# Performance work log

Hardware: AMD Instinct MI355X
Metric: run time of the kernel (lower is better)

## Reference

```python
import jax, jax.numpy as jnp
import numpy as np

N, E, H, NUM_RBF = 50000, 800000, 32, 32
D_IN = 2 * (NUM_RBF + H)  # 128: att_src(H) + att_dst(H) + rbf(2*NUM_RBF)
LN_EPS = 1e-5


def _decompose(t):
    # irreducible decomposition of [..., 3, 3] tensor
    eye = jnp.eye(3, dtype=t.dtype)
    I = jnp.mean(jnp.diagonal(t, axis1=-2, axis2=-1), axis=-1)[..., None, None] * eye
    A = 0.5 * (t - jnp.swapaxes(t, -1, -2))
    S = 0.5 * (t + jnp.swapaxes(t, -1, -2)) - I
    return I, A, S


def _tnorm(t):
    # squared Frobenius norm over last two dims -> [..., H]
    return (t ** 2).sum((-2, -1))


def _chan_lin(t, W):
    # nn.Linear over channel dim: t [N,H,3,3], W [H_out,H_in]
    return jnp.einsum('nhij,gh->ngij', t, W)


def setup_inputs() -> dict:
    key = jax.random.key(0)
    ks = jax.random.split(key, 12)

    def lin(k, o, i):
        return (jax.random.normal(k, (o, i), jnp.float32) / np.sqrt(i)).astype(jnp.float32)

    return {
        'X': jax.random.normal(ks[0], (N, H, 3, 3), jnp.float32),
        'rbf': jax.random.normal(ks[1], (E, 2 * NUM_RBF), jnp.float32),
        'dist': jax.random.uniform(ks[2], (E,), jnp.float32),
        'src': jax.random.randint(ks[3], (E,), 0, N),
        'dst': jax.random.randint(ks[4], (E,), 0, N),
        'Ws0': lin(ks[5], H, D_IN), 'b0': jnp.zeros((H,), jnp.float32),
        'Ws1': lin(ks[6], 2 * H, H), 'b1': jnp.zeros((2 * H,), jnp.float32),
        'Ws2': lin(ks[7], 3 * H, 2 * H), 'b2': jnp.zeros((3 * H,), jnp.float32),
        'Wt': (jax.random.normal(ks[8], (6, H, H), jnp.float32) / np.sqrt(H)).astype(jnp.float32),
        'ln_w': jnp.ones((3 * H,), jnp.float32), 'ln_b': jnp.zeros((3 * H,), jnp.float32),
        'lin_w': lin(ks[9], H, 3 * H), 'lin_b': jnp.zeros((H,), jnp.float32),
    }


def reference(X, rbf, dist, src, dst, Ws0, b0, Ws1, b1, Ws2, b2, Wt, ln_w, ln_b, lin_w, lin_b):
    n = X.shape[0]
    act = jax.nn.silu

    # atom_inf branch: per-node scalar attributes from tensor norms
    I, A, S = _decompose(X)
    x = jnp.concatenate([_tnorm(I), _tnorm(A), _tnorm(S)], axis=-1)  # [N, 3H]
    mu = x.mean(-1, keepdims=True)
    var = x.var(-1, keepdims=True)
    x = (x - mu) / jnp.sqrt(var + LN_EPS) * ln_w + ln_b
    att = act(x @ lin_w.T + lin_b)  # [N, H]

    # edge features: cat(att[src], att[dst], rbf) -> scalar MLP
    e = jnp.concatenate([att[src], att[dst], rbf], axis=-1)  # [E, D_IN]
    e = act(e @ Ws0.T + b0)
    e = act(e @ Ws1.T + b1)
    e = act(e @ Ws2.T + b2)  # [E, 3H]
    C = jnp.ones_like(dist)  # original code overwrites cutoff with ones
    e = (e * C[:, None]).reshape(e.shape[0], H, 3)  # [E, H, 3]

    # normalize node tensors, decompose, per-channel linear mix
    Xn = X / (_tnorm(X) + 1.0)[..., None, None]
    I, A, S = _decompose(Xn)
    I = _chan_lin(I, Wt[0])
    A = _chan_lin(A, Wt[1])
    S = _chan_lin(S, Wt[2])
    Y = I + A + S

    # tensor message passing: gather src, scale by edge factor, scatter-sum to dst
    def mp(T, f):
        return jax.ops.segment_sum(T[src] * f[:, :, None, None], dst, num_segments=n)

    msg = mp(I, e[..., 0]) + mp(A, e[..., 1]) + mp(S, e[..., 2])

    # O(3) group
    B1 = jnp.matmul(msg, Y)
    B2 = jnp.matmul(Y, msg)
    I, A, S = _decompose(B1 + B2)

    normp1 = (_tnorm(I + A + S) + 1.0)[..., None, None]
    I, A, S = I / normp1, A / normp1, S / normp1
    I = _chan_lin(I, Wt[3])
    A = _chan_lin(A, Wt[4])
    S = _chan_lin(S, Wt[5])
    dX = I + A + S
    X_out = Xn + dX + jnp.matmul(dX, dX)  # matrix_power(dX, 2)
    return X_out, e
```

## Files before the change

kernel.cpp:

```cpp
#include <hip/hip_runtime.h>
#include <math.h>

#define HC 32
#define NODE_PER_BLK 8

typedef _Float16 half8 __attribute__((ext_vector_type(8)));
typedef float float4v __attribute__((ext_vector_type(4)));

__device__ __forceinline__ float silu_f(float x) { return x / (1.0f + __expf(-x)); }

__device__ __forceinline__ unsigned int pk2(float a, float b) {
    union { _Float16 h[2]; unsigned int u; } t;
    t.h[0] = (_Float16)a; t.h[1] = (_Float16)b;
    return t.u;
}
__device__ __forceinline__ void unpk2(unsigned int u, float& a, float& b) {
    union { unsigned int u; _Float16 h[2]; } t;
    t.u = u;
    a = (float)t.h[0]; b = (float)t.h[1];
}

__device__ __forceinline__ void recon3(const float* c, float* T) {
    T[0] = c[0] + c[4];  T[1] = c[1] + c[5];  T[2] = c[2] + c[6];
    T[3] = -c[1] + c[5]; T[4] = c[0] + c[7];  T[5] = c[3] + c[8];
    T[6] = -c[2] + c[6]; T[7] = -c[3] + c[8]; T[8] = c[0] - c[4] - c[7];
}

__global__ void prep_weights(const float* __restrict__ Ws0, const float* __restrict__ Ws1,
                             const float* __restrict__ Ws2,
                             _Float16* __restrict__ wf1, _Float16* __restrict__ wf2,
                             _Float16* __restrict__ wf3) {
    int t = blockIdx.x * 256 + threadIdx.x;
    int j = t & 7;
    int lane = (t >> 3) & 63;
    int q = lane >> 4, r = lane & 15;
    if (t < 4096) {
        int fi = t >> 9, kt = fi >> 1, nt = fi & 1;
        wf1[t] = (_Float16)Ws0[(16 * nt + r) * 128 + 32 * kt + 8 * q + j];
    } else if (t < 6144) {
        int t2 = t - 4096;
        int nt = t2 >> 9;
        wf2[t2] = (_Float16)Ws1[(16 * nt + r) * 32 + 8 * q + j];
    } else if (t < 12288) {
        int t3 = t - 6144;
        int fi = t3 >> 9, kt = fi / 6, nt = fi % 6;
        wf3[t3] = (_Float16)Ws2[(16 * nt + r) * 64 + 32 * kt + 8 * q + j];
    }
}

__global__ void hist_kernel(const int* __restrict__ dst, int* __restrict__ cnt, int E) {
    int e = blockIdx.x * 256 + threadIdx.x;
    if (e < E) atomicAdd(&cnt[dst[e]], 1);
}

__global__ __launch_bounds__(1024) void scan_a(const int* __restrict__ cnt,
                                               int* __restrict__ bsum, int N) {
    __shared__ int s[1024];
    int i = blockIdx.x * 1024 + threadIdx.x;
    s[threadIdx.x] = (i < N) ? cnt[i] : 0;
    __syncthreads();
    #pragma unroll
    for (int o = 512; o; o >>= 1) {
        if (threadIdx.x < o) s[threadIdx.x] += s[threadIdx.x + o];
        __syncthreads();
    }
    if (threadIdx.x == 0) bsum[blockIdx.x] = s[0];
}

__global__ __launch_bounds__(1024) void scan_b(int* __restrict__ bsum, int nb) {
    __shared__ int s[1024];
    int v = (threadIdx.x < nb) ? bsum[threadIdx.x] : 0;
    s[threadIdx.x] = v;
    __syncthreads();
    #pragma unroll
    for (int o = 1; o < 1024; o <<= 1) {
        int t = (threadIdx.x >= o) ? s[threadIdx.x - o] : 0;
        __syncthreads();
        s[threadIdx.x] += t;
        __syncthreads();
    }
    if (threadIdx.x < nb) bsum[threadIdx.x] = s[threadIdx.x] - v;
}

__global__ __launch_bounds__(1024) void scan_c(const int* __restrict__ cnt,
                                               const int* __restrict__ bsum,
                                               int* __restrict__ off,
                                               int* __restrict__ cursor, int N) {
    __shared__ int s[1024];
    int i = blockIdx.x * 1024 + threadIdx.x;
    int v = (i < N) ? cnt[i] : 0;
    s[threadIdx.x] = v;
    __syncthreads();
    #pragma unroll
    for (int o = 1; o < 1024; o <<= 1) {
        int t = (threadIdx.x >= o) ? s[threadIdx.x - o] : 0;
        __syncthreads();
        s[threadIdx.x] += t;
        __syncthreads();
    }
    int ex = bsum[blockIdx.x] + s[threadIdx.x] - v;
    if (i < N) {
        off[i] = ex;
        cursor[i] = ex;
        if (i == N - 1) off[N] = ex + v;
    }
}

__global__ void scatter_kernel(const int* __restrict__ src, const int* __restrict__ dst,
                               int* __restrict__ cursor, int2* __restrict__ elist, int E) {
    int e = blockIdx.x * 256 + threadIdx.x;
    if (e >= E) return;
    int d = dst[e];
    int pos = atomicAdd(&cursor[d], 1);
    elist[pos] = make_int2(e, src[e]);
}

__global__ void node_prep(const float* __restrict__ X,
                          const float* __restrict__ lin_w, const float* __restrict__ lin_b,
                          const float* __restrict__ ln_w, const float* __restrict__ ln_b,
                          const float* __restrict__ Wt,
                          float* __restrict__ att, unsigned int* __restrict__ comp_g, int N) {
    __shared__ float sX[NODE_PER_BLK][96];
    __shared__ float sC[NODE_PER_BLK][HC * 9];
    int grp = threadIdx.x >> 5;
    int lane = threadIdx.x & 31;
    int n = blockIdx.x * NODE_PER_BLK + grp;
    bool valid = (n < N);

    float m = 0, a01 = 0, a02 = 0, a12 = 0, s00 = 0, s01 = 0, s02 = 0, s11 = 0, s12 = 0, s22 = 0;
    float tI = 0, tA = 0, tS = 0, tX = 0;
    if (valid) {
        const float* xp = X + (size_t)n * 288 + lane * 9;
        float t00 = xp[0], t01 = xp[1], t02 = xp[2];
        float t10 = xp[3], t11 = xp[4], t12 = xp[5];
        float t20 = xp[6], t21 = xp[7], t22 = xp[8];
        m = (t00 + t11 + t22) * (1.0f / 3.0f);
        a01 = 0.5f * (t01 - t10); a02 = 0.5f * (t02 - t20); a12 = 0.5f * (t12 - t21);
        s00 = t00 - m; s11 = t11 - m; s22 = t22 - m;
        s01 = 0.5f * (t01 + t10); s02 = 0.5f * (t02 + t20); s12 = 0.5f * (t12 + t21);
        tI = 3.0f * m * m;
        tA = 2.0f * (a01 * a01 + a02 * a02 + a12 * a12);
        tS = s00 * s00 + s11 * s11 + s22 * s22 + 2.0f * (s01 * s01 + s02 * s02 + s12 * s12);
        tX = tI + tA + tS;
    }
    float lsum = tI + tA + tS;
    #pragma unroll
    for (int o = 16; o; o >>= 1) lsum += __shfl_xor(lsum, o, 32);
    float mu = lsum * (1.0f / 96.0f);
    float d0 = tI - mu, d1 = tA - mu, d2 = tS - mu;
    float lsq = d0 * d0 + d1 * d1 + d2 * d2;
    #pragma unroll
    for (int o = 16; o; o >>= 1) lsq += __shfl_xor(lsq, o, 32);
    float rstd = rsqrtf(lsq * (1.0f / 96.0f) + 1e-5f);
    if (valid) {
        sX[grp][lane]      = d0 * rstd * ln_w[lane]      + ln_b[lane];
        sX[grp][32 + lane] = d1 * rstd * ln_w[32 + lane] + ln_b[32 + lane];
        sX[grp][64 + lane] = d2 * rstd * ln_w[64 + lane] + ln_b[64 + lane];
    }
    __syncthreads();
    if (valid) {
        float acc = lin_b[lane];
        const float* wr = lin_w + lane * 96;
        #pragma unroll
        for (int k = 0; k < 96; k++) acc += wr[k] * sX[grp][k];
        att[(size_t)n * 32 + lane] = silu_f(acc);
        float inv = 1.0f / (tX + 1.0f);
        float* cc = &sC[grp][lane * 9];
        cc[0] = m * inv;
        cc[1] = a01 * inv; cc[2] = a02 * inv; cc[3] = a12 * inv;
        cc[4] = s00 * inv; cc[5] = s01 * inv; cc[6] = s02 * inv;
        cc[7] = s11 * inv; cc[8] = s12 * inv;
    }
    __syncthreads();
    if (valid) {
        float o[9];
        #pragma unroll
        for (int c = 0; c < 9; c++) o[c] = 0.0f;
        const float* w0 = Wt + lane * 32;
        const float* w1 = Wt + 1024 + lane * 32;
        const float* w2 = Wt + 2048 + lane * 32;
        #pragma unroll
        for (int h = 0; h < 32; h++) {
            float wi = w0[h], wa = w1[h], ws = w2[h];
            const float* ch = &sC[grp][h * 9];
            o[0] += wi * ch[0];
            o[1] += wa * ch[1]; o[2] += wa * ch[2]; o[3] += wa * ch[3];
            o[4] += ws * ch[4]; o[5] += ws * ch[5]; o[6] += ws * ch[6];
            o[7] += ws * ch[7]; o[8] += ws * ch[8];
        }
        unsigned int* cgp = comp_g + (size_t)n * 160 + lane;
        cgp[0]   = pk2(o[0], o[1]);
        cgp[32]  = pk2(o[2], o[3]);
        cgp[64]  = pk2(o[4], o[5]);
        cgp[96]  = pk2(o[6], o[7]);
        cgp[128] = pk2(o[8], 0.0f);
    }
}

__device__ __forceinline__ half8 cvt8(const float* p) {
    half8 h;
    #pragma unroll
    for (int j = 0; j < 8; j++) h[j] = (_Float16)p[j];
    return h;
}

__global__ __launch_bounds__(256) void edge_mfma(
    const float* __restrict__ att, const float* __restrict__ rbf,
    const int* __restrict__ src, const int* __restrict__ dst,
    const _Float16* __restrict__ wf1, const _Float16* __restrict__ wf2,
    const _Float16* __restrict__ wf3,
    const float* __restrict__ b0, const float* __restrict__ b1, const float* __restrict__ b2,
    float* __restrict__ e_out, int E) {
    __shared__ _Float16 hbuf[4][16][72];
    int w = threadIdx.x >> 6;
    int lane = threadIdx.x & 63;
    int q = lane >> 4, r = lane & 15;
    int ebase = blockIdx.x * 64 + w * 16;
    int er = min(ebase + r, E - 1);
    int s = src[er], d = dst[er];

    half8 a0 = cvt8(att + (size_t)s * 32 + 8 * q);
    half8 a1 = cvt8(att + (size_t)d * 32 + 8 * q);
    half8 a2 = cvt8(rbf + (size_t)er * 64 + 8 * q);
    half8 a3 = cvt8(rbf + (size_t)er * 64 + 32 + 8 * q);

    const half8* W1 = (const half8*)wf1;
    float bn0 = b0[r], bn1 = b0[16 + r];
    float4v acc10 = {bn0, bn0, bn0, bn0};
    float4v acc11 = {bn1, bn1, bn1, bn1};
    acc10 = __builtin_amdgcn_mfma_f32_16x16x32_f16(a0, W1[0 * 64 + lane], acc10, 0, 0, 0);
    acc11 = __builtin_amdgcn_mfma_f32_16x16x32_f16(a0, W1[1 * 64 + lane], acc11, 0, 0, 0);
    acc10 = __builtin_amdgcn_mfma_f32_16x16x32_f16(a1, W1[2 * 64 + lane], acc10, 0, 0, 0);
    acc11 = __builtin_amdgcn_mfma_f32_16x16x32_f16(a1, W1[3 * 64 + lane], acc11, 0, 0, 0);
    acc10 = __builtin_amdgcn_mfma_f32_16x16x32_f16(a2, W1[4 * 64 + lane], acc10, 0, 0, 0);
    acc11 = __builtin_amdgcn_mfma_f32_16x16x32_f16(a2, W1[5 * 64 + lane], acc11, 0, 0, 0);
    acc10 = __builtin_amdgcn_mfma_f32_16x16x32_f16(a3, W1[6 * 64 + lane], acc10, 0, 0, 0);
    acc11 = __builtin_amdgcn_mfma_f32_16x16x32_f16(a3, W1[7 * 64 + lane], acc11, 0, 0, 0);
    #pragma unroll
    for (int reg = 0; reg < 4; reg++) {
        hbuf[w][4 * q + reg][r]      = (_Float16)silu_f(acc10[reg]);
        hbuf[w][4 * q + reg][16 + r] = (_Float16)silu_f(acc11[reg]);
    }

    half8 ah1 = *(const half8*)&hbuf[w][r][8 * q];
    const half8* W2 = (const half8*)wf2;
    float4v acc2[4];
    #pragma unroll
    for (int nt = 0; nt < 4; nt++) {
        float bb = b1[16 * nt + r];
        acc2[nt] = (float4v){bb, bb, bb, bb};
        acc2[nt] = __builtin_amdgcn_mfma_f32_16x16x32_f16(ah1, W2[nt * 64 + lane], acc2[nt], 0, 0, 0);
    }
    #pragma unroll
    for (int nt = 0; nt < 4; nt++) {
        #pragma unroll
        for (int reg = 0; reg < 4; reg++) {
            hbuf[w][4 * q + reg][16 * nt + r] = (_Float16)silu_f(acc2[nt][reg]);
        }
    }

    half8 ah20 = *(const half8*)&hbuf[w][r][8 * q];
    half8 ah21 = *(const half8*)&hbuf[w][r][32 + 8 * q];
    const half8* W3 = (const half8*)wf3;
    float4v acc3[6];
    #pragma unroll
    for (int nt = 0; nt < 6; nt++) {
        float bb = b2[16 * nt + r];
        acc3[nt] = (float4v){bb, bb, bb, bb};
        acc3[nt] = __builtin_amdgcn_mfma_f32_16x16x32_f16(ah20, W3[nt * 64 + lane], acc3[nt], 0, 0, 0);
        acc3[nt] = __builtin_amdgcn_mfma_f32_16x16x32_f16(ah21, W3[(6 + nt) * 64 + lane], acc3[nt], 0, 0, 0);
    }
    #pragma unroll
    for (int nt = 0; nt < 6; nt++) {
        #pragma unroll
        for (int reg = 0; reg < 4; reg++) {
            int ee = ebase + 4 * q + reg;
            if (ee < E) e_out[(size_t)ee * 96 + 16 * nt + r] = silu_f(acc3[nt][reg]);
        }
    }
}

__global__ __launch_bounds__(256) void gather_final(
    const float* __restrict__ X, const unsigned int* __restrict__ comp_g,
    const float* __restrict__ e_out,
    const int* __restrict__ off, const int2* __restrict__ elist,
    const float* __restrict__ Wt, float* __restrict__ Xout, int N) {
    __shared__ float sM[8][288];
    __shared__ float sB[288];
    int n = blockIdx.x;
    int grp = threadIdx.x >> 5;
    int lane = threadIdx.x & 31;
    int start = off[n], end = off[n + 1];

    float cm[9];
    #pragma unroll
    for (int c = 0; c < 9; c++) cm[c] = 0.0f;

    for (int idx = start + grp; idx < end; idx += 8) {
        int2 es = elist[idx];
        const float* ep = e_out + (size_t)es.x * 96 + lane * 3;
        float e0 = ep[0], e1 = ep[1], e2 = ep[2];
        const unsigned int* cg = comp_g + (size_t)es.y * 160 + lane;
        float c0, c1, c2, c3, c4, c5, c6, c7, c8, cz;
        unpk2(cg[0], c0, c1);
        unpk2(cg[32], c2, c3);
        unpk2(cg[64], c4, c5);
        unpk2(cg[96], c6, c7);
        unpk2(cg[128], c8, cz);
        cm[0] += e0 * c0;
        cm[1] += e1 * c1; cm[2] += e1 * c2; cm[3] += e1 * c3;
        cm[4] += e2 * c4; cm[5] += e2 * c5; cm[6] += e2 * c6;
        cm[7] += e2 * c7; cm[8] += e2 * c8;
    }
    #pragma unroll
    for (int c = 0; c < 9; c++) sM[grp][lane * 9 + c] = cm[c];
    __syncthreads();
    for (int t = threadIdx.x; t < 288; t += 256) {
        float s = sM[0][t];
        #pragma unroll
        for (int g = 1; g < 8; g++) s += sM[g][t];
        sM[0][t] = s;
    }
    __syncthreads();

    if (grp == 0) {
        float cmt[9];
        #pragma unroll
        for (int c = 0; c < 9; c++) cmt[c] = sM[0][lane * 9 + c];
        float cy[9], cz;
        const unsigned int* cgn = comp_g + (size_t)n * 160 + lane;
        unpk2(cgn[0], cy[0], cy[1]);
        unpk2(cgn[32], cy[2], cy[3]);
        unpk2(cgn[64], cy[4], cy[5]);
        unpk2(cgn[96], cy[6], cy[7]);
        unpk2(cgn[128], cy[8], cz);
        float M[9], Y[9];
        recon3(cmt, M);
        recon3(cy, Y);
        float B[9];
        #pragma unroll
        for (int i = 0; i < 3; i++) {
            #pragma unroll
            for (int j = 0; j < 3; j++) {
                float acc = 0.0f;
                #pragma unroll
                for (int k = 0; k < 3; k++)
                    acc += M[i * 3 + k] * Y[k * 3 + j] + Y[i * 3 + k] * M[k * 3 + j];
                B[i * 3 + j] = acc;
            }
        }
        float mB = (B[0] + B[4] + B[8]) * (1.0f / 3.0f);
        float tn = 1.0f;
        #pragma unroll
        for (int i = 0; i < 9; i++) tn += B[i] * B[i];
        float itn = 1.0f / tn;
        float* bb = &sB[lane * 9];
        bb[0] = mB * itn;
        bb[1] = 0.5f * (B[1] - B[3]) * itn;
        bb[2] = 0.5f * (B[2] - B[6]) * itn;
        bb[3] = 0.5f * (B[5] - B[7]) * itn;
        bb[4] = (B[0] - mB) * itn;
        bb[5] = 0.5f * (B[1] + B[3]) * itn;
        bb[6] = 0.5f * (B[2] + B[6]) * itn;
        bb[7] = (B[4] - mB) * itn;
        bb[8] = 0.5f * (B[5] + B[7]) * itn;
    }
    __syncthreads();
    if (grp == 0) {
        float o[9];
        #pragma unroll
        for (int c = 0; c < 9; c++) o[c] = 0.0f;
        const float* w3 = Wt + 3 * 1024 + lane * 32;
        const float* w4 = Wt + 4 * 1024 + lane * 32;
        const float* w5 = Wt + 5 * 1024 + lane * 32;
        #pragma unroll
        for (int h = 0; h < 32; h++) {
            float wi = w3[h], wa = w4[h], ws = w5[h];
            const float* ch = &sB[h * 9];
            o[0] += wi * ch[0];
            o[1] += wa * ch[1]; o[2] += wa * ch[2]; o[3] += wa * ch[3];
            o[4] += ws * ch[4]; o[5] += ws * ch[5]; o[6] += ws * ch[6];
            o[7] += ws * ch[7]; o[8] += ws * ch[8];
        }
        float D[9];
        recon3(o, D);
        const float* xp = X + (size_t)n * 288 + lane * 9;
        float xv[9];
        float tt = 0.0f;
        #pragma unroll
        for (int i = 0; i < 9; i++) { xv[i] = xp[i]; tt += xv[i] * xv[i]; }
        float inv = 1.0f / (tt + 1.0f);
        float P[9];
        #pragma unroll
        for (int i = 0; i < 3; i++) {
            #pragma unroll
            for (int j = 0; j < 3; j++) {
                float acc = 0.0f;
                #pragma unroll
                for (int k = 0; k < 3; k++) acc += D[i * 3 + k] * D[k * 3 + j];
                P[i * 3 + j] = acc;
            }
        }
        float* op = Xout + (size_t)n * 288 + lane * 9;
        #pragma unroll
        for (int i = 0; i < 9; i++) op[i] = xv[i] * inv + D[i] + P[i];
    }
}

extern "C" void kernel_launch(void* const* d_in, const int* in_sizes, int n_in,
                              void* d_out, int out_size, void* d_ws, size_t ws_size,
                              hipStream_t stream) {
    const float* X = (const float*)d_in[0];
    const float* rbf = (const float*)d_in[1];
    const int* src = (const int*)d_in[3];
    const int* dst = (const int*)d_in[4];
    const float* Ws0 = (const float*)d_in[5];
    const float* b0 = (const float*)d_in[6];
    const float* Ws1 = (const float*)d_in[7];
    const float* b1 = (const float*)d_in[8];
    const float* Ws2 = (const float*)d_in[9];
    const float* b2 = (const float*)d_in[10];
    const float* Wt = (const float*)d_in[11];
    const float* ln_w = (const float*)d_in[12];
    const float* ln_b = (const float*)d_in[13];
    const float* lin_w = (const float*)d_in[14];
    const float* lin_b = (const float*)d_in[15];

    int N = in_sizes[0] / 288;
    int E = in_sizes[1] / 64;

    float* Xout = (float*)d_out;
    float* e_out = (float*)d_out + (size_t)N * 288;

    float* att = (float*)d_ws;
    unsigned int* comp_g = (unsigned int*)(att + (size_t)N * 32);
    _Float16* wf1 = (_Float16*)(comp_g + (size_t)N * 160);
    _Float16* wf2 = wf1 + 4096;
    _Float16* wf3 = wf2 + 2048;
    int* cnt = (int*)(wf3 + 6144);
    int* off = cnt + N;
    int* cursor = off + N + 1;
    int* bsum = cursor + N + 1;
    int2* elist = (int2*)(bsum + 1026);

    int nb = (N + 1023) / 1024;

    hipMemsetAsync(cnt, 0, (size_t)N * sizeof(int), stream);
    prep_weights<<<48, 256, 0, stream>>>(Ws0, Ws1, Ws2, wf1, wf2, wf3);
    node_prep<<<(N + NODE_PER_BLK - 1) / NODE_PER_BLK, 256, 0, stream>>>(
        X, lin_w, lin_b, ln_w, ln_b, Wt, att, comp_g, N);
    hist_kernel<<<(E + 255) / 256, 256, 0, stream>>>(dst, cnt, E);
    scan_a<<<nb, 1024, 0, stream>>>(cnt, bsum, N);
    scan_b<<<1, 1024, 0, stream>>>(bsum, nb);
    scan_c<<<nb, 1024, 0, stream>>>(cnt, bsum, off, cursor, N);
    scatter_kernel<<<(E + 255) / 256, 256, 0, stream>>>(src, dst, cursor, elist, E);
    edge_mfma<<<(E + 63) / 64, 256, 0, stream>>>(
        att, rbf, src, dst, wf1, wf2, wf3, b0, b1, b2, e_out, E);
    gather_final<<<N, 256, 0, stream>>>(
        X, comp_g, e_out, off, elist, Wt, Xout, N);
}
```

Baseline: 665.9 us.

## Process one node per 32-lane group in gather kernel and vectorize edge input loads

Result: faster. 574.2 us (-13.8%).

```diff
diff --git a/kernel.cpp b/kernel.cpp
--- a/kernel.cpp
+++ b/kernel.cpp
@@ -197,10 +197,12 @@
     }
 }
 
-__device__ __forceinline__ half8 cvt8(const float* p) {
+__device__ __forceinline__ half8 cvt8v(const float* p) {
+    float4 v0 = ((const float4*)p)[0];
+    float4 v1 = ((const float4*)p)[1];
     half8 h;
-    #pragma unroll
-    for (int j = 0; j < 8; j++) h[j] = (_Float16)p[j];
+    h[0] = (_Float16)v0.x; h[1] = (_Float16)v0.y; h[2] = (_Float16)v0.z; h[3] = (_Float16)v0.w;
+    h[4] = (_Float16)v1.x; h[5] = (_Float16)v1.y; h[6] = (_Float16)v1.z; h[7] = (_Float16)v1.w;
     return h;
 }
 
@@ -219,10 +221,10 @@
     int er = min(ebase + r, E - 1);
     int s = src[er], d = dst[er];
 
-    half8 a0 = cvt8(att + (size_t)s * 32 + 8 * q);
-    half8 a1 = cvt8(att + (size_t)d * 32 + 8 * q);
-    half8 a2 = cvt8(rbf + (size_t)er * 64 + 8 * q);
-    half8 a3 = cvt8(rbf + (size_t)er * 64 + 32 + 8 * q);
+    half8 a0 = cvt8v(att + (size_t)s * 32 + 8 * q);
+    half8 a1 = cvt8v(att + (size_t)d * 32 + 8 * q);
+    half8 a2 = cvt8v(rbf + (size_t)er * 64 + 8 * q);
+    half8 a3 = cvt8v(rbf + (size_t)er * 64 + 32 + 8 * q);
 
     const half8* W1 = (const half8*)wf1;
     float bn0 = b0[r], bn1 = b0[16 + r];
@@ -285,48 +287,70 @@
     const float* __restrict__ e_out,
     const int* __restrict__ off, const int2* __restrict__ elist,
     const float* __restrict__ Wt, float* __restrict__ Xout, int N) {
-    __shared__ float sM[8][288];
-    __shared__ float sB[288];
-    int n = blockIdx.x;
+    __shared__ float sB[NODE_PER_BLK][HC * 9];
     int grp = threadIdx.x >> 5;
     int lane = threadIdx.x & 31;
-    int start = off[n], end = off[n + 1];
+    int n = blockIdx.x * NODE_PER_BLK + grp;
+    bool valid = (n < N);
 
     float cm[9];
     #pragma unroll
     for (int c = 0; c < 9; c++) cm[c] = 0.0f;
 
-    for (int idx = start + grp; idx < end; idx += 8) {
-        int2 es = elist[idx];
-        const float* ep = e_out + (size_t)es.x * 96 + lane * 3;
-        float e0 = ep[0], e1 = ep[1], e2 = ep[2];
-        const unsigned int* cg = comp_g + (size_t)es.y * 160 + lane;
-        float c0, c1, c2, c3, c4, c5, c6, c7, c8, cz;
-        unpk2(cg[0], c0, c1);
-        unpk2(cg[32], c2, c3);
-        unpk2(cg[64], c4, c5);
-        unpk2(cg[96], c6, c7);
-        unpk2(cg[128], c8, cz);
-        cm[0] += e0 * c0;
-        cm[1] += e1 * c1; cm[2] += e1 * c2; cm[3] += e1 * c3;
-        cm[4] += e2 * c4; cm[5] += e2 * c5; cm[6] += e2 * c6;
-        cm[7] += e2 * c7; cm[8] += e2 * c8;
-    }
-    #pragma unroll
-    for (int c = 0; c < 9; c++) sM[grp][lane * 9 + c] = cm[c];
-    __syncthreads();
-    for (int t = threadIdx.x; t < 288; t += 256) {
-        float s = sM[0][t];
-        #pragma unroll
-        for (int g = 1; g < 8; g++) s += sM[g][t];
-        sM[0][t] = s;
-    }
-    __syncthreads();
-
-    if (grp == 0) {
-        float cmt[9];
-        #pragma unroll
-        for (int c = 0; c < 9; c++) cmt[c] = sM[0][lane * 9 + c];
+    if (valid) {
+        int start = off[n], end = off[n + 1];
+        int idx = start;
+        for (; idx + 4 <= end; idx += 4) {
+            int ex[4], sx[4];
+            #pragma unroll
+            for (int u = 0; u < 4; u++) {
+                int2 es = elist[idx + u];
+                ex[u] = es.x; sx[u] = es.y;
+            }
+            float ev[4][3];
+            unsigned int cg[4][5];
+            #pragma unroll
+            for (int u = 0; u < 4; u++) {
+                const float* ep = e_out + (size_t)ex[u] * 96 + lane * 3;
+                ev[u][0] = ep[0]; ev[u][1] = ep[1]; ev[u][2] = ep[2];
+                const unsigned int* cp = comp_g + (size_t)sx[u] * 160 + lane;
+                cg[u][0] = cp[0]; cg[u][1] = cp[32]; cg[u][2] = cp[64];
+                cg[u][3] = cp[96]; cg[u][4] = cp[128];
+            }
+            #pragma unroll
+            for (int u = 0; u < 4; u++) {
+                float c0, c1, c2, c3, c4, c5, c6, c7, c8, cz;
+                unpk2(cg[u][0], c0, c1);
+                unpk2(cg[u][1], c2, c3);
+                unpk2(cg[u][2], c4, c5);
+                unpk2(cg[u][3], c6, c7);
+                unpk2(cg[u][4], c8, cz);
+                float e0 = ev[u][0], e1 = ev[u][1], e2 = ev[u][2];
+                cm[0] += e0 * c0;
+                cm[1] += e1 * c1; cm[2] += e1 * c2; cm[3] += e1 * c3;
+                cm[4] += e2 * c4; cm[5] += e2 * c5; cm[6] += e2 * c6;
+                cm[7] += e2 * c7; cm[8] += e2 * c8;
+            }
+        }
+        for (; idx < end; idx++) {
+            int2 es = elist[idx];
+            const float* ep = e_out + (size_t)es.x * 96 + lane * 3;
+            float e0 = ep[0], e1 = ep[1], e2 = ep[2];
+            const unsigned int* cp = comp_g + (size_t)es.y * 160 + lane;
+            float c0, c1, c2, c3, c4, c5, c6, c7, c8, cz;
+            unpk2(cp[0], c0, c1);
+            unpk2(cp[32], c2, c3);
+            unpk2(cp[64], c4, c5);
+            unpk2(cp[96], c6, c7);
+            unpk2(cp[128], c8, cz);
+            cm[0] += e0 * c0;
+            cm[1] += e1 * c1; cm[2] += e1 * c2; cm[3] += e1 * c3;
+            cm[4] += e2 * c4; cm[5] += e2 * c5; cm[6] += e2 * c6;
+            cm[7] += e2 * c7; cm[8] += e2 * c8;
+        }
+    }
+
+    if (valid) {
         float cy[9], cz;
         const unsigned int* cgn = comp_g + (size_t)n * 160 + lane;
         unpk2(cgn[0], cy[0], cy[1]);
@@ -335,7 +359,7 @@
         unpk2(cgn[96], cy[6], cy[7]);
         unpk2(cgn[128], cy[8], cz);
         float M[9], Y[9];
-        recon3(cmt, M);
+        recon3(cm, M);
         recon3(cy, Y);
         float B[9];
         #pragma unroll
@@ -354,7 +378,7 @@
         #pragma unroll
         for (int i = 0; i < 9; i++) tn += B[i] * B[i];
         float itn = 1.0f / tn;
-        float* bb = &sB[lane * 9];
+        float* bb = &sB[grp][lane * 9];
         bb[0] = mB * itn;
         bb[1] = 0.5f * (B[1] - B[3]) * itn;
         bb[2] = 0.5f * (B[2] - B[6]) * itn;
@@ -366,7 +390,7 @@
         bb[8] = 0.5f * (B[5] + B[7]) * itn;
     }
     __syncthreads();
-    if (grp == 0) {
+    if (valid) {
         float o[9];
         #pragma unroll
         for (int c = 0; c < 9; c++) o[c] = 0.0f;
@@ -376,7 +400,7 @@
         #pragma unroll
         for (int h = 0; h < 32; h++) {
             float wi = w3[h], wa = w4[h], ws = w5[h];
-            const float* ch = &sB[h * 9];
+            const float* ch = &sB[grp][h * 9];
             o[0] += wi * ch[0];
             o[1] += wa * ch[1]; o[2] += wa * ch[2]; o[3] += wa * ch[3];
             o[4] += ws * ch[4]; o[5] += ws * ch[5]; o[6] += ws * ch[6];
@@ -456,6 +480,6 @@
     scatter_kernel<<<(E + 255) / 256, 256, 0, stream>>>(src, dst, cursor, elist, E);
     edge_mfma<<<(E + 63) / 64, 256, 0, stream>>>(
         att, rbf, src, dst, wf1, wf2, wf3, b0, b1, b2, e_out, E);
-    gather_final<<<N, 256, 0, stream>>>(
+    gather_final<<<(N + NODE_PER_BLK - 1) / NODE_PER_BLK, 256, 0, stream>>>(
         X, comp_g, e_out, off, elist, Wt, Xout, N);
 }
```
